# Kernel tuning notes

Hardware: AMD Instinct MI355X
Metric: run time of the kernel (lower is better)

Reference implementation:

```python
import jax, jax.numpy as jnp
import numpy as np

EMBED = 3072
NQ = 32
NKV = 8
HD = EMBED // NQ  # 96
GROUPS = NQ // NKV  # 4
ROPE_BASE = 10000.0


def apply_rope(t, positions):
    # t: [b, h, s, d]; positions: [s] int
    d = t.shape[-1]
    inv_freq = 1.0 / (ROPE_BASE ** (jnp.arange(0, d, 2, dtype=jnp.float32) / d))  # [d/2]
    ang = positions.astype(jnp.float32)[:, None] * inv_freq[None, :]  # [s, d/2]
    cos = jnp.cos(ang)[None, None]  # [1,1,s,d/2]
    sin = jnp.sin(ang)[None, None]
    t1, t2 = t[..., : d // 2], t[..., d // 2 :]
    return jnp.concatenate([t1 * cos - t2 * sin, t2 * cos + t1 * sin], axis=-1)


def setup_inputs() -> dict:
    key = jax.random.key(0)
    k1, k2, k3 = jax.random.split(key, 3)
    b, s = 2, 2048
    x = jax.random.normal(k1, (b, s, EMBED), dtype=jnp.float32)
    positions = jnp.arange(s, dtype=jnp.int32)
    mask = jnp.triu(jnp.ones((s, s), dtype=bool), k=1)  # True = masked (causal)
    qkv_size = NQ * HD + 2 * NKV * HD  # 4608
    W_qkv = jax.random.normal(k2, (qkv_size, EMBED), dtype=jnp.float32) * (EMBED ** -0.5)
    W_o = jax.random.normal(k3, (EMBED, EMBED), dtype=jnp.float32) * (EMBED ** -0.5)
    return {"x": x, "positions": positions, "mask": mask, "W_qkv": W_qkv, "W_o": W_o}


def reference(x, positions, mask, W_qkv, W_o):
    b, s, _ = x.shape
    scaling = HD ** -0.5
    qkv = x @ W_qkv.T  # [b, s, 4608]
    q_size, kv_size = NQ * HD, NKV * HD
    q = qkv[..., :q_size].reshape(b, s, NQ, HD).transpose(0, 2, 1, 3)          # [b,NQ,s,d]
    k = qkv[..., q_size : q_size + kv_size].reshape(b, s, NKV, HD).transpose(0, 2, 1, 3)
    v = qkv[..., q_size + kv_size :].reshape(b, s, NKV, HD).transpose(0, 2, 1, 3)
    q = apply_rope(q, positions)
    k = apply_rope(k, positions)
    q = q.reshape(b, NKV, GROUPS, s, HD)
    scores = jnp.einsum("bkgsd,bktd->bkgst", q, k) * scaling  # [b,NKV,G,s,s]
    scores = jnp.where(mask[None, None, None], -jnp.inf, scores)
    attn = jax.nn.softmax(scores, axis=-1)
    out = jnp.einsum("bkgst,bktd->bkgsd", attn, v)
    out = out.reshape(b, NQ, s, HD).transpose(0, 2, 1, 3).reshape(b, s, NQ * HD)
    return out @ W_o.T
```

## Files before the change

kernel.cpp:

```cpp
#include <hip/hip_runtime.h>
#include <cstdint>

typedef unsigned short u16;
typedef unsigned int u32;
typedef __attribute__((ext_vector_type(4))) float f32x4;
typedef __attribute__((ext_vector_type(8))) __bf16 bf16x8;
typedef __attribute__((ext_vector_type(8))) unsigned short u16x8;
typedef __attribute__((ext_vector_type(4))) unsigned int u32x4;

#define S_LEN 2048
#define BATCH 2
#define NQH 32
#define NKVH 8
#define HD 96
#define EMB 3072
#define QKVN 4608
#define KOFF 3072
#define VOFF 3840

__device__ __forceinline__ u16 f2b(float f) {
    u32 u = __float_as_uint(f);
    u32 r = (u + 0x7fffu + ((u >> 16) & 1u)) >> 16;
    return (u16)r;
}
__device__ __forceinline__ float b2f(u16 h) { return __uint_as_float(((u32)h) << 16); }
__device__ __forceinline__ u32 pk2(float a, float b) {
    return (u32)f2b(a) | ((u32)f2b(b) << 16);
}

__global__ __launch_bounds__(256) void conv_f2b(const float* __restrict__ in,
                                                u16* __restrict__ outp, int n8) {
    const int i = blockIdx.x * 256 + threadIdx.x;
    if (i >= n8) return;
    const f32x4* q = (const f32x4*)(in + (size_t)i * 8);
    const f32x4 a = q[0], b = q[1];
    u16x8 t;
#pragma unroll
    for (int j = 0; j < 4; ++j) {
        t[j] = f2b(a[j]);
        t[j + 4] = f2b(b[j]);
    }
    *(u16x8*)(outp + (size_t)i * 8) = t;
}

template <bool F32>
__device__ __forceinline__ bf16x8 load_frag8(const void* base, size_t elem) {
    if constexpr (F32) {
        const f32x4* q = (const f32x4*)((const float*)base + elem);
        const f32x4 a = q[0], b = q[1];
        u16x8 t;
#pragma unroll
        for (int i = 0; i < 4; ++i) {
            t[i] = f2b(a[i]);
            t[i + 4] = f2b(b[i]);
        }
        return __builtin_bit_cast(bf16x8, t);
    } else {
        return *(const bf16x8*)((const u16*)base + elem);
    }
}

template <bool AF32, bool BF32, bool OUTF32>
__global__ __launch_bounds__(256) void gqa_gemm_bt(const void* __restrict__ Ap,
                                                   const void* __restrict__ Bp,
                                                   void* __restrict__ Cp,
                                                   int M, int N, int K) {
    __shared__ __align__(16) u16 As[128 * 32];
    __shared__ __align__(16) u16 Bs[128 * 32];
    const int tid = threadIdx.x;
    const int wave = tid >> 6, lane = tid & 63;
    const int bm = blockIdx.y * 128, bn = blockIdx.x * 128;
    const int wm = (wave >> 1) * 64, wn = (wave & 1) * 64;
    const int lrow = lane & 15, lk = (lane >> 4) * 8;
    const int ra = tid >> 2, ca = (tid & 3) * 8;
    const int rb = (tid + 256) >> 2, cb = (tid & 3) * 8;
    f32x4 acc[4][4] = {};

    for (int k0 = 0; k0 < K; k0 += 32) {
        const bf16x8 a0 = load_frag8<AF32>(Ap, (size_t)(bm + ra) * K + k0 + ca);
        const bf16x8 a1 = load_frag8<AF32>(Ap, (size_t)(bm + rb) * K + k0 + cb);
        const bf16x8 b0 = load_frag8<BF32>(Bp, (size_t)(bn + ra) * K + k0 + ca);
        const bf16x8 b1 = load_frag8<BF32>(Bp, (size_t)(bn + rb) * K + k0 + cb);
        __syncthreads();
        *(bf16x8*)(As + ra * 32 + ca) = a0;
        *(bf16x8*)(As + rb * 32 + cb) = a1;
        *(bf16x8*)(Bs + ra * 32 + ca) = b0;
        *(bf16x8*)(Bs + rb * 32 + cb) = b1;
        __syncthreads();
        bf16x8 af[4], bfr[4];
#pragma unroll
        for (int mi = 0; mi < 4; ++mi)
            af[mi] = *(const bf16x8*)(As + (wm + mi * 16 + lrow) * 32 + lk);
#pragma unroll
        for (int ni = 0; ni < 4; ++ni)
            bfr[ni] = *(const bf16x8*)(Bs + (wn + ni * 16 + lrow) * 32 + lk);
#pragma unroll
        for (int mi = 0; mi < 4; ++mi)
#pragma unroll
            for (int ni = 0; ni < 4; ++ni)
                acc[mi][ni] = __builtin_amdgcn_mfma_f32_16x16x32_bf16(af[mi], bfr[ni],
                                                                      acc[mi][ni], 0, 0, 0);
    }
    const int orow = bm + wm + (lane >> 4) * 4;
    const int ocol = bn + wn + lrow;
#pragma unroll
    for (int mi = 0; mi < 4; ++mi)
#pragma unroll
        for (int ni = 0; ni < 4; ++ni)
#pragma unroll
            for (int r = 0; r < 4; ++r) {
                const size_t idx = (size_t)(orow + mi * 16 + r) * N + ocol + ni * 16;
                if constexpr (OUTF32)
                    ((float*)Cp)[idx] = acc[mi][ni][r];
                else
                    ((u16*)Cp)[idx] = f2b(acc[mi][ni][r]);
            }
}

__global__ __launch_bounds__(256) void gqa_rope(u16* __restrict__ qkv,
                                                const int* __restrict__ positions) {
    int i = blockIdx.x * 256 + threadIdx.x;
    const int pair = i % 48;
    int t = i / 48;
    const int head = t % (NQH + NKVH);
    const int bs = t / (NQH + NKVH);
    const int pos = positions[bs & (S_LEN - 1)];
    const size_t base = (size_t)bs * QKVN + (head < NQH ? head * HD : KOFF + (head - NQH) * HD);
    const float invf = __expf(-(float)(2 * pair) * (1.0f / 96.0f) * 9.210340371976184f);
    const float ang = (float)pos * invf;
    float sn, cs;
    __sincosf(ang, &sn, &cs);
    const float t1 = b2f(qkv[base + pair]);
    const float t2 = b2f(qkv[base + 48 + pair]);
    qkv[base + pair] = f2b(t1 * cs - t2 * sn);
    qkv[base + 48 + pair] = f2b(t2 * cs + t1 * sn);
}

__global__ __launch_bounds__(256) void gqa_attn3(const u16* __restrict__ qkv,
                                                 u16* __restrict__ out) {
    __shared__ __align__(16) u16 Ks[64 * 96];
    __shared__ __align__(16) u16 Vt[96 * 72];

    const int tid = threadIdx.x;
    const int wave = tid >> 6, lane = tid & 63;
    const int lrow = lane & 15, lhi = lane >> 4;
    const int bx = blockIdx.x;
    const int qt32 = 63 - (bx >> 4);
    const int kvh = (bx >> 1) & 7, bb = bx & 1;
    const int qh = kvh * 4 + wave;
    const int srow0 = bb * S_LEN + qt32 * 32;
    const int kb_last = (qt32 * 32 + 31) >> 6;
    const float cl2 = 0.10206207261596575f * 1.4426950408889634f;

    bf16x8 bq[2][3];
#pragma unroll
    for (int qt = 0; qt < 2; ++qt)
#pragma unroll
        for (int kd = 0; kd < 3; ++kd)
            bq[qt][kd] = *(const bf16x8*)(qkv + (size_t)(srow0 + qt * 16 + lrow) * QKVN +
                                          qh * 96 + kd * 32 + lhi * 8);

    float m_s[2] = {-3e38f, -3e38f}, l_s[2] = {0.0f, 0.0f};
    f32x4 oacc[6][2] = {};

    const int s0 = lrow + ((lane & 16) ? 32 : 0);
    const int s1 = s0 + 16;
    const bool khi = (lane & 32) != 0;

    const size_t kvrow0 = (size_t)(bb * S_LEN) * QKVN;
    for (int kb = 0; kb <= kb_last; ++kb) {
        __syncthreads();
        const size_t kbase = kvrow0 + (size_t)(kb * 64) * QKVN + KOFF + kvh * 96;
        const size_t vbase = kvrow0 + (size_t)(kb * 64) * QKVN + VOFF + kvh * 96;
        for (int u = tid; u < 768; u += 256) {
            const int oct = u % 12, row = u / 12;
            *(u16x8*)(Ks + row * 96 + oct * 8) =
                *(const u16x8*)(qkv + kbase + (size_t)row * QKVN + oct * 8);
        }
        for (int u = tid; u < 768; u += 256) {
            const int d = u % 96, so8 = u / 96;
            u16x8 v8;
#pragma unroll
            for (int j = 0; j < 8; ++j) v8[j] = qkv[vbase + (size_t)(so8 * 8 + j) * QKVN + d];
            *(u16x8*)(Vt + d * 72 + so8 * 8) = v8;
        }
        __syncthreads();

        bf16x8 ka[4][3];
#pragma unroll
        for (int kt = 0; kt < 4; ++kt)
#pragma unroll
            for (int kd = 0; kd < 3; ++kd)
                ka[kt][kd] = *(const bf16x8*)(Ks + (kt * 16 + lrow) * 96 + kd * 32 + lhi * 8);

        const int qoff = qt32 * 32 - kb * 64;
        const bool lastkb = (kb == kb_last);
        u32 bp[2][2][4];

#pragma unroll
        for (int qt = 0; qt < 2; ++qt) {
            const int qrelmax = qoff + qt * 16 + 15;
            f32x4 sacc[4] = {};
#pragma unroll
            for (int kt = 0; kt < 4; ++kt) {
                if (lastkb && kt * 16 > qrelmax) continue;
#pragma unroll
                for (int kd = 0; kd < 3; ++kd)
                    sacc[kt] = __builtin_amdgcn_mfma_f32_16x16x32_bf16(ka[kt][kd], bq[qt][kd],
                                                                       sacc[kt], 0, 0, 0);
            }
            float p[4][4];
            float mx = -3e38f;
            if (lastkb) {
                const int qrel = qoff + qt * 16 + lrow;
#pragma unroll
                for (int kt = 0; kt < 4; ++kt)
#pragma unroll
                    for (int r = 0; r < 4; ++r) {
                        const bool live = (kt * 16 + lhi * 4 + r) <= qrel;
                        const float s = live ? sacc[kt][r] : -3e38f;
                        p[kt][r] = s;
                        mx = fmaxf(mx, s);
                    }
            } else {
#pragma unroll
                for (int kt = 0; kt < 4; ++kt)
#pragma unroll
                    for (int r = 0; r < 4; ++r) {
                        p[kt][r] = sacc[kt][r];
                        mx = fmaxf(mx, sacc[kt][r]);
                    }
            }
            mx = fmaxf(mx, __shfl_xor(mx, 16));
            mx = fmaxf(mx, __shfl_xor(mx, 32));
            const float mn = fmaxf(m_s[qt], mx);
            const float alpha = exp2f((m_s[qt] - mn) * cl2);
            m_s[qt] = mn;
            float rs = 0.0f;
#pragma unroll
            for (int kt = 0; kt < 4; ++kt)
#pragma unroll
                for (int r = 0; r < 4; ++r) {
                    const float pv = exp2f((p[kt][r] - mn) * cl2);
                    p[kt][r] = pv;
                    rs += pv;
                }
            rs += __shfl_xor(rs, 16);
            rs += __shfl_xor(rs, 32);
            l_s[qt] = l_s[qt] * alpha + rs;
#pragma unroll
            for (int dt = 0; dt < 6; ++dt)
#pragma unroll
                for (int r = 0; r < 4; ++r) oacc[dt][qt][r] *= alpha;
            u32 pk[4][2];
#pragma unroll
            for (int kt = 0; kt < 4; ++kt) {
                pk[kt][0] = pk2(p[kt][0], p[kt][1]);
                pk[kt][1] = pk2(p[kt][2], p[kt][3]);
            }
#pragma unroll
            for (int kk = 0; kk < 2; ++kk) {
                const u32 a0 = (u32)__shfl((int)pk[kk * 2][0], s0, 64);
                const u32 b0 = (u32)__shfl((int)pk[kk * 2 + 1][0], s0, 64);
                const u32 a1 = (u32)__shfl((int)pk[kk * 2][1], s0, 64);
                const u32 b1 = (u32)__shfl((int)pk[kk * 2 + 1][1], s0, 64);
                const u32 a2 = (u32)__shfl((int)pk[kk * 2][0], s1, 64);
                const u32 b2 = (u32)__shfl((int)pk[kk * 2 + 1][0], s1, 64);
                const u32 a3 = (u32)__shfl((int)pk[kk * 2][1], s1, 64);
                const u32 b3 = (u32)__shfl((int)pk[kk * 2 + 1][1], s1, 64);
                bp[qt][kk][0] = khi ? b0 : a0;
                bp[qt][kk][1] = khi ? b1 : a1;
                bp[qt][kk][2] = khi ? b2 : a2;
                bp[qt][kk][3] = khi ? b3 : a3;
            }
        }

#pragma unroll
        for (int dt = 0; dt < 6; ++dt) {
            bf16x8 va[2];
#pragma unroll
            for (int kk = 0; kk < 2; ++kk)
                va[kk] = *(const bf16x8*)(Vt + (dt * 16 + lrow) * 72 + kk * 32 + lhi * 8);
#pragma unroll
            for (int qt = 0; qt < 2; ++qt)
#pragma unroll
                for (int kk = 0; kk < 2; ++kk) {
                    const u32x4 bv = {bp[qt][kk][0], bp[qt][kk][1], bp[qt][kk][2], bp[qt][kk][3]};
                    oacc[dt][qt] = __builtin_amdgcn_mfma_f32_16x16x32_bf16(
                        va[kk], __builtin_bit_cast(bf16x8, bv), oacc[dt][qt], 0, 0, 0);
                }
        }
    }

    const size_t obase = (size_t)srow0 * EMB + qh * 96;
#pragma unroll
    for (int qt = 0; qt < 2; ++qt) {
        const float inv = 1.0f / l_s[qt];
        const size_t rbase = obase + (size_t)(qt * 16 + lrow) * EMB;
#pragma unroll
        for (int dt = 0; dt < 6; ++dt)
#pragma unroll
            for (int rp = 0; rp < 2; ++rp) {
                const u32 pair = pk2(oacc[dt][qt][2 * rp] * inv, oacc[dt][qt][2 * rp + 1] * inv);
                *(u32*)(out + rbase + dt * 16 + lhi * 4 + 2 * rp) = pair;
            }
    }
}

extern "C" void kernel_launch(void* const* d_in, const int* in_sizes, int n_in,
                              void* d_out, int out_size, void* d_ws, size_t ws_size,
                              hipStream_t stream) {
    const float* x = (const float*)d_in[0];
    const int* positions = (const int*)d_in[1];
    const float* W_qkv = (const float*)d_in[3];
    const float* W_o = (const float*)d_in[4];
    float* out = (float*)d_out;

    const int M = BATCH * S_LEN;
    const size_t QKV_E = (size_t)M * QKVN;
    const size_t ATT_E = (size_t)M * EMB;
    const size_t X_E = (size_t)M * EMB;
    const size_t WQ_E = (size_t)QKVN * EMB;
    const size_t WO_E = (size_t)EMB * EMB;

    u16* qkv_ws = (u16*)d_ws;
    u16* attn_ws = qkv_ws + QKV_E;
    u16* xb = attn_ws + ATT_E;
    u16* wqb = xb + X_E;
    u16* wob = wqb + WQ_E;
    const size_t need = (QKV_E + ATT_E + X_E + WQ_E + WO_E) * 2;

    if (ws_size >= need) {
        conv_f2b<<<(int)(X_E / 8 + 255) / 256, 256, 0, stream>>>(x, xb, (int)(X_E / 8));
        conv_f2b<<<(int)(WQ_E / 8 + 255) / 256, 256, 0, stream>>>(W_qkv, wqb, (int)(WQ_E / 8));
        conv_f2b<<<(int)(WO_E / 8 + 255) / 256, 256, 0, stream>>>(W_o, wob, (int)(WO_E / 8));
        gqa_gemm_bt<false, false, false>
            <<<dim3(QKVN / 128, M / 128), 256, 0, stream>>>(xb, wqb, qkv_ws, M, QKVN, EMB);
        gqa_rope<<<(BATCH * S_LEN * (NQH + NKVH) * 48) / 256, 256, 0, stream>>>(qkv_ws, positions);
        gqa_attn3<<<dim3(1024), 256, 0, stream>>>(qkv_ws, attn_ws);
        gqa_gemm_bt<false, false, true>
            <<<dim3(EMB / 128, M / 128), 256, 0, stream>>>(attn_ws, wob, out, M, EMB, EMB);
    } else {
        gqa_gemm_bt<true, true, false>
            <<<dim3(QKVN / 128, M / 128), 256, 0, stream>>>(x, W_qkv, qkv_ws, M, QKVN, EMB);
        gqa_rope<<<(BATCH * S_LEN * (NQH + NKVH) * 48) / 256, 256, 0, stream>>>(qkv_ws, positions);
        gqa_attn3<<<dim3(1024), 256, 0, stream>>>(qkv_ws, attn_ws);
        gqa_gemm_bt<false, true, true>
            <<<dim3(EMB / 128, M / 128), 256, 0, stream>>>(attn_ws, W_o, out, M, EMB, EMB);
    }
}
```

Measured before the change: 665.6 us.

## Add LDS-staged GEMM, lazy softmax rescaling, and hardware bf16 packing

Both projection GEMMs move to a new kernel that copies 128x32 A and B tiles into shared memory with global_load_lds, so all four waves reuse the same tile before running MFMAs. The attention softmax now skips rescaling of the running max and output accumulator unless some lane's max grows by more than a threshold, which removes most per-tile exp and multiply work. Float-to-bf16 packing uses the v_cvt_pk_bf16_f32 instruction in place of the software rounding routine. The new GEMM is single-buffered with two barriers per K step, so load latency is not overlapped. Its epilogue also writes scalar values with a strided pattern, which may cost more than the old store path.

```diff
diff --git a/kernel.cpp b/kernel.cpp
--- a/kernel.cpp
+++ b/kernel.cpp
@@ -24,8 +24,10 @@
     return (u16)r;
 }
 __device__ __forceinline__ float b2f(u16 h) { return __uint_as_float(((u32)h) << 16); }
-__device__ __forceinline__ u32 pk2(float a, float b) {
-    return (u32)f2b(a) | ((u32)f2b(b) << 16);
+__device__ __forceinline__ u32 cvtpk(float lo, float hi) {
+    u32 r;
+    asm("v_cvt_pk_bf16_f32 %0, %1, %2" : "=v"(r) : "v"(lo), "v"(hi));
+    return r;
 }
 
 __global__ __launch_bounds__(256) void conv_f2b(const float* __restrict__ in,
@@ -41,6 +43,75 @@
         t[j + 4] = f2b(b[j]);
     }
     *(u16x8*)(outp + (size_t)i * 8) = t;
+}
+
+typedef __attribute__((address_space(1))) const uint32_t gas_u32;
+typedef __attribute__((address_space(3))) uint32_t las_u32;
+__device__ __forceinline__ void gld_lds16(const u16* g, u16* l) {
+    __builtin_amdgcn_global_load_lds((gas_u32*)g, (las_u32*)l, 16, 0, 0);
+}
+
+template <bool OUTF32>
+__global__ __launch_bounds__(256) void gemm_bt_lds(const u16* __restrict__ Ap,
+                                                   const u16* __restrict__ Bp,
+                                                   void* __restrict__ Cp,
+                                                   int M, int N, int K) {
+    __shared__ __align__(16) u16 As[128 * 32];
+    __shared__ __align__(16) u16 Bs[128 * 32];
+    const int tid = threadIdx.x;
+    const int wave = tid >> 6, lane = tid & 63;
+    const int bm = blockIdx.y * 128, bn = blockIdx.x * 128;
+    const int wm = (wave >> 1) * 64, wn = (wave & 1) * 64;
+    const int lrow = lane & 15, lk = (lane >> 4) * 8;
+
+    const int seg = (tid & 3) * 8;
+    const int r0 = tid >> 2;
+    const u16* gA0 = Ap + (size_t)(bm + r0) * K + seg;
+    const u16* gA1 = Ap + (size_t)(bm + r0 + 64) * K + seg;
+    const u16* gB0 = Bp + (size_t)(bn + r0) * K + seg;
+    const u16* gB1 = Bp + (size_t)(bn + r0 + 64) * K + seg;
+    const int wbase = (tid & 192) * 8;
+    u16* lA0 = As + wbase;
+    u16* lA1 = As + wbase + 2048;
+    u16* lB0 = Bs + wbase;
+    u16* lB1 = Bs + wbase + 2048;
+
+    f32x4 acc[4][4] = {};
+    for (int k0 = 0; k0 < K; k0 += 32) {
+        __syncthreads();
+        gld_lds16(gA0 + k0, lA0);
+        gld_lds16(gA1 + k0, lA1);
+        gld_lds16(gB0 + k0, lB0);
+        gld_lds16(gB1 + k0, lB1);
+        __syncthreads();
+        bf16x8 af[4], bfr[4];
+#pragma unroll
+        for (int mi = 0; mi < 4; ++mi)
+            af[mi] = *(const bf16x8*)(As + (wm + mi * 16 + lrow) * 32 + lk);
+#pragma unroll
+        for (int ni = 0; ni < 4; ++ni)
+            bfr[ni] = *(const bf16x8*)(Bs + (wn + ni * 16 + lrow) * 32 + lk);
+#pragma unroll
+        for (int mi = 0; mi < 4; ++mi)
+#pragma unroll
+            for (int ni = 0; ni < 4; ++ni)
+                acc[mi][ni] = __builtin_amdgcn_mfma_f32_16x16x32_bf16(af[mi], bfr[ni],
+                                                                      acc[mi][ni], 0, 0, 0);
+    }
+    const int orow = bm + wm + (lane >> 4) * 4;
+    const int ocol = bn + wn + lrow;
+#pragma unroll
+    for (int mi = 0; mi < 4; ++mi)
+#pragma unroll
+        for (int ni = 0; ni < 4; ++ni)
+#pragma unroll
+            for (int r = 0; r < 4; ++r) {
+                const size_t idx = (size_t)(orow + mi * 16 + r) * N + ocol + ni * 16;
+                if constexpr (OUTF32)
+                    ((float*)Cp)[idx] = acc[mi][ni][r];
+                else
+                    ((u16*)Cp)[idx] = f2b(acc[mi][ni][r]);
+            }
 }
 
 template <bool F32>
@@ -233,9 +304,18 @@
             }
             mx = fmaxf(mx, __shfl_xor(mx, 16));
             mx = fmaxf(mx, __shfl_xor(mx, 32));
-            const float mn = fmaxf(m_s[qt], mx);
-            const float alpha = exp2f((m_s[qt] - mn) * cl2);
-            m_s[qt] = mn;
+            float mn = m_s[qt];
+            if (!__all(mx - mn <= 20.0f)) {
+                const float mnew = fmaxf(mn, mx);
+                const float alpha = exp2f((mn - mnew) * cl2);
+                m_s[qt] = mnew;
+                mn = mnew;
+                l_s[qt] *= alpha;
+#pragma unroll
+                for (int dt = 0; dt < 6; ++dt)
+#pragma unroll
+                    for (int r = 0; r < 4; ++r) oacc[dt][qt][r] *= alpha;
+            }
             float rs = 0.0f;
 #pragma unroll
             for (int kt = 0; kt < 4; ++kt)
@@ -247,16 +327,12 @@
                 }
             rs += __shfl_xor(rs, 16);
             rs += __shfl_xor(rs, 32);
-            l_s[qt] = l_s[qt] * alpha + rs;
-#pragma unroll
-            for (int dt = 0; dt < 6; ++dt)
-#pragma unroll
-                for (int r = 0; r < 4; ++r) oacc[dt][qt][r] *= alpha;
+            l_s[qt] += rs;
             u32 pk[4][2];
 #pragma unroll
             for (int kt = 0; kt < 4; ++kt) {
-                pk[kt][0] = pk2(p[kt][0], p[kt][1]);
-                pk[kt][1] = pk2(p[kt][2], p[kt][3]);
+                pk[kt][0] = cvtpk(p[kt][0], p[kt][1]);
+                pk[kt][1] = cvtpk(p[kt][2], p[kt][3]);
             }
 #pragma unroll
             for (int kk = 0; kk < 2; ++kk) {
@@ -301,7 +377,7 @@
         for (int dt = 0; dt < 6; ++dt)
 #pragma unroll
             for (int rp = 0; rp < 2; ++rp) {
-                const u32 pair = pk2(oacc[dt][qt][2 * rp] * inv, oacc[dt][qt][2 * rp + 1] * inv);
+                const u32 pair = cvtpk(oacc[dt][qt][2 * rp] * inv, oacc[dt][qt][2 * rp + 1] * inv);
                 *(u32*)(out + rbase + dt * 16 + lhi * 4 + 2 * rp) = pair;
             }
     }
@@ -334,11 +410,11 @@
         conv_f2b<<<(int)(X_E / 8 + 255) / 256, 256, 0, stream>>>(x, xb, (int)(X_E / 8));
         conv_f2b<<<(int)(WQ_E / 8 + 255) / 256, 256, 0, stream>>>(W_qkv, wqb, (int)(WQ_E / 8));
         conv_f2b<<<(int)(WO_E / 8 + 255) / 256, 256, 0, stream>>>(W_o, wob, (int)(WO_E / 8));
-        gqa_gemm_bt<false, false, false>
+        gemm_bt_lds<false>
             <<<dim3(QKVN / 128, M / 128), 256, 0, stream>>>(xb, wqb, qkv_ws, M, QKVN, EMB);
         gqa_rope<<<(BATCH * S_LEN * (NQH + NKVH) * 48) / 256, 256, 0, stream>>>(qkv_ws, positions);
         gqa_attn3<<<dim3(1024), 256, 0, stream>>>(qkv_ws, attn_ws);
-        gqa_gemm_bt<false, false, true>
+        gemm_bt_lds<true>
             <<<dim3(EMB / 128, M / 128), 256, 0, stream>>>(attn_ws, wob, out, M, EMB, EMB);
     } else {
         gqa_gemm_bt<true, true, false>
```

Measured after the change: 643.6 us. 3.3% less time.
